# Optimization experiments

Measured on AMD Instinct MI355X. Metric: run time of the kernel, lower is better.

Reference implementation:

```python
import jax, jax.numpy as jnp
import numpy as np
from jax import lax


def _conv(x, w, b):
    # NCHW conv, 3x3, stride 1, SAME padding (matches nn.Conv2d(k=3, padding=1))
    y = lax.conv_general_dilated(x, w, (1, 1), 'SAME',
                                 dimension_numbers=('NCHW', 'OIHW', 'NCHW'))
    return y + b[None, :, None, None]


def _maxpool2(x):
    return lax.reduce_window(x, -jnp.inf, lax.max, (1, 1, 2, 2), (1, 1, 2, 2), 'VALID')


def setup_inputs() -> dict:
    key = jax.random.key(0)
    ks = jax.random.split(key, 8)
    B, C, H, W = 512, 3, 32, 32
    E, NC = 4, 100
    x = jax.random.normal(ks[0], (B, C, H, W), jnp.float32)
    s = lambda k, shape, fan: jax.random.normal(k, shape, jnp.float32) * (1.0 / np.sqrt(fan))
    return {
        'x': x,
        'r_conv_w': s(ks[1], (16, 3, 3, 3), 27),
        'r_conv_b': jnp.zeros((16,), jnp.float32),
        'r_fc_w': s(ks[2], (E, 16), 16),
        'r_fc_b': jnp.zeros((E,), jnp.float32),
        'e_w1': s(ks[3], (E, 32, 3, 3, 3), 27),
        'e_b1': jnp.zeros((E, 32), jnp.float32),
        'e_w2': s(ks[4], (E, 64, 32, 3, 3), 32 * 9),
        'e_b2': jnp.zeros((E, 64), jnp.float32),
        'e_fc_w': s(ks[5], (E, NC, 64 * 8 * 8), 64 * 8 * 8),
        'e_fc_b': jnp.zeros((E, NC), jnp.float32),
        'top_k': 1,
    }


def reference(x, r_conv_w, r_conv_b, r_fc_w, r_fc_b,
              e_w1, e_b1, e_w2, e_b2, e_fc_w, e_fc_b, top_k):
    E = r_fc_w.shape[0]
    # ---- router: conv -> relu -> global avg pool -> linear -> softmax ----
    h = jax.nn.relu(_conv(x, r_conv_w, r_conv_b))
    g = h.mean(axis=(2, 3))                                   # [B, 16]
    router_probs = jax.nn.softmax(g @ r_fc_w.T + r_fc_b, -1)   # [B, E]
    topk_prob, topk_idx = lax.top_k(router_probs, top_k)       # [B, K]

    # ---- experts (dense compute + weighted combine == hard dispatch/combine) ----
    def expert(w1, b1, w2, b2, fw, fb):
        h1 = _maxpool2(jax.nn.relu(_conv(x, w1, b1)))          # [B, 32, 16, 16]
        h2 = _maxpool2(jax.nn.relu(_conv(h1, w2, b2)))         # [B, 64, 8, 8]
        f = h2.reshape(h2.shape[0], -1)                        # [B, 4096]
        return f @ fw.T + fb                                   # [B, NC]

    expert_out = jax.vmap(expert)(e_w1, e_b1, e_w2, e_b2, e_fc_w, e_fc_b)  # [E, B, NC]

    onehot = jax.nn.one_hot(topk_idx, E, dtype=x.dtype)        # [B, K, E]
    comb_w = jnp.einsum('bke,bk->be', onehot, topk_prob)       # [B, E]
    final_output = jnp.einsum('ebc,be->bc', expert_out, comb_w)

    mean_probs = router_probs.mean(axis=0)
    aux_loss = jnp.mean((mean_probs - 1.0 / E) ** 2)
    return final_output, router_probs, aux_loss
```

## Files before the change

kernel.cpp:

```cpp
#include <hip/hip_runtime.h>
#include <hip/hip_bf16.h>
#include <math.h>

#define BATCH 512
#define NC 100

typedef __attribute__((ext_vector_type(8))) short bf16x8;
typedef __attribute__((ext_vector_type(4))) float f32x4;

__device__ inline ushort f2bf(float f) {
    __hip_bfloat16 h = __float2bfloat16(f);
    return *reinterpret_cast<ushort*>(&h);
}

__global__ __launch_bounds__(256) void cvt_all_kernel(const float* __restrict__ fw,
                                                      ushort* __restrict__ fwb,
                                                      const float* __restrict__ w2,
                                                      ushort* __restrict__ w2t,
                                                      const float* __restrict__ w1,
                                                      ushort* __restrict__ w1t)
{
    const int blk = blockIdx.x;
    if (blk < 1600) {
        const int i = (blk * 256 + threadIdx.x) * 4;
        float4 v = *(const float4*)(fw + i);
        ushort o[4];
        o[0] = f2bf(v.x); o[1] = f2bf(v.y); o[2] = f2bf(v.z); o[3] = f2bf(v.w);
        *(uint2*)(fwb + i) = *(uint2*)o;
    } else if (blk < 1888) {
        const int i = (blk - 1600) * 256 + threadIdx.x;
        const int ic = i & 31;
        const int oc = (i >> 5) & 63;
        const int et = i >> 11;
        const int e = et / 9, t = et % 9;
        w2t[i] = f2bf(w2[((e * 64 + oc) * 32 + ic) * 9 + t]);
    } else {
        const int i = (blk - 1888) * 256 + threadIdx.x;
        const int row = i >> 5, k = i & 31;
        w1t[i] = (k < 27) ? f2bf(w1[row * 27 + k]) : (ushort)0;
    }
}

__global__ __launch_bounds__(512) void fused_expert_kernel(
    const float* __restrict__ x,
    const float* __restrict__ rcw,
    const float* __restrict__ rcb,
    const float* __restrict__ rfw,
    const float* __restrict__ rfb,
    const ushort* __restrict__ w1t,
    const float* __restrict__ eb1,
    const ushort* __restrict__ w2t,
    const float* __restrict__ eb2,
    float* __restrict__ probs_out,
    int* __restrict__ sel,
    float* __restrict__ pw,
    uint* __restrict__ h2b)
{
    __shared__ float xs[3 * 34 * 40];
    __shared__ float rcb_s[16];
    __shared__ float rfw_s[68];
    __shared__ float red[8][16];
    __shared__ float g_s[16];
    __shared__ int   sel_s;
    __shared__ float eb1_s[128];
    __shared__ __align__(16) ushort A_s[18 * 18 * 32];

    const int b = blockIdx.x, tid = threadIdx.x;
    const int wvv = tid >> 6, lane = tid & 63;
    const int lr = lane & 15, kb = lane >> 4;

    uint* A32 = (uint*)A_s;
    for (int i = tid; i < 1088; i += 512) {
        int y, xx, w;
        if (i < 576) { y = (i >= 288) ? 17 : 0; int r2 = i % 288; xx = r2 >> 4; w = r2 & 15; }
        else { int j = i - 576; y = 1 + (j >> 5); xx = ((j >> 4) & 1) ? 17 : 0; w = j & 15; }
        A32[(y * 18 + xx) * 16 + w] = 0u;
    }
    for (int i = tid; i < 3 * 34 * 40; i += 512) xs[i] = 0.f;
    if (tid < 128) eb1_s[tid] = eb1[tid];
    if (tid < 68) rfw_s[tid] = (tid < 64) ? rfw[tid] : rfb[tid - 64];
    if (tid >= 128 && tid < 144) rcb_s[tid - 128] = rcb[tid - 128];
    __syncthreads();
    const float* xb = x + b * 3072;
    for (int i = tid; i < 3072; i += 512) {
        int c = i >> 10, r = (i >> 5) & 31, cc = i & 31;
        xs[(c * 34 + r + 1) * 40 + (cc + 1)] = xb[i];
    }
    __syncthreads();

    {
        const int oc = tid & 15, sg = tid >> 4;
        const int pg = sg & 15, half = sg >> 4;
        const int c0 = half * 16;
        float w[27];
#pragma unroll
        for (int j = 0; j < 27; ++j) w[j] = rcw[oc * 27 + j];
        const float bias = rcb_s[oc];
        float a0[16], a1[16];
#pragma unroll
        for (int j = 0; j < 16; ++j) { a0[j] = 0.f; a1[j] = 0.f; }
#pragma unroll
        for (int c = 0; c < 3; ++c) {
#pragma unroll
            for (int ry = 0; ry < 4; ++ry) {
                const float* row = &xs[(c * 34 + 2 * pg + ry) * 40 + c0];
                float rv[18];
                float4 q0 = *(const float4*)(row);
                float4 q1 = *(const float4*)(row + 4);
                float4 q2 = *(const float4*)(row + 8);
                float4 q3 = *(const float4*)(row + 12);
                float2 q4 = *(const float2*)(row + 16);
                rv[0] = q0.x; rv[1] = q0.y; rv[2] = q0.z; rv[3] = q0.w;
                rv[4] = q1.x; rv[5] = q1.y; rv[6] = q1.z; rv[7] = q1.w;
                rv[8] = q2.x; rv[9] = q2.y; rv[10] = q2.z; rv[11] = q2.w;
                rv[12] = q3.x; rv[13] = q3.y; rv[14] = q3.z; rv[15] = q3.w;
                rv[16] = q4.x; rv[17] = q4.y;
                if (ry < 3) {
#pragma unroll
                    for (int kx = 0; kx < 3; ++kx) {
                        const float wv = w[c * 9 + ry * 3 + kx];
#pragma unroll
                        for (int j = 0; j < 16; ++j) a0[j] += wv * rv[j + kx];
                    }
                }
                if (ry > 0) {
#pragma unroll
                    for (int kx = 0; kx < 3; ++kx) {
                        const float wv = w[c * 9 + (ry - 1) * 3 + kx];
#pragma unroll
                        for (int j = 0; j < 16; ++j) a1[j] += wv * rv[j + kx];
                    }
                }
            }
        }
        float accm = 0.f;
#pragma unroll
        for (int j = 0; j < 16; ++j)
            accm += fmaxf(a0[j] + bias, 0.f) + fmaxf(a1[j] + bias, 0.f);
        accm += __shfl_down(accm, 32);
        accm += __shfl_down(accm, 16);
        if (lane < 16) red[wvv][lane] = accm;
    }
    __syncthreads();
    if (tid < 16) {
        float s = 0.f;
#pragma unroll
        for (int w = 0; w < 8; ++w) s += red[w][tid];
        g_s[tid] = s * (1.f / 1024.f);
    }
    __syncthreads();

    if (tid == 0) {
        float logits[4];
#pragma unroll
        for (int e = 0; e < 4; ++e) {
            float s = rfw_s[64 + e];
#pragma unroll
            for (int o = 0; o < 16; ++o) s += g_s[o] * rfw_s[e * 16 + o];
            logits[e] = s;
        }
        float m = fmaxf(fmaxf(logits[0], logits[1]), fmaxf(logits[2], logits[3]));
        float ex[4], ssum = 0.f;
#pragma unroll
        for (int e = 0; e < 4; ++e) { ex[e] = __expf(logits[e] - m); ssum += ex[e]; }
        const float inv = 1.f / ssum;
        float p[4];
#pragma unroll
        for (int e = 0; e < 4; ++e) p[e] = ex[e] * inv;
        int am = 0; float best = p[0];
#pragma unroll
        for (int e = 1; e < 4; ++e) { if (p[e] > best) { best = p[e]; am = e; } }
        *(float4*)(probs_out + b * 4) = make_float4(p[0], p[1], p[2], p[3]);
        sel[b] = am;
        pw[b] = best;
        sel_s = am;
    }
    __syncthreads();
    const int e = sel_s;

    {
        const ushort* bsrc = w1t + (e * 32 + lr) * 32 + kb * 8;
        const bf16x8 b0 = *(const bf16x8*)(bsrc);
        const bf16x8 b1 = *(const bf16x8*)(bsrc + 16 * 32);
        const float bv0 = eb1_s[e * 32 + lr];
        const float bv1 = eb1_s[e * 32 + 16 + lr];

        int offj[8], valj[8];
#pragma unroll
        for (int jj = 0; jj < 8; ++jj) {
            int k = kb * 8 + jj;
            int ic = (k * 57) >> 9; ic = ic > 2 ? 2 : ic;
            int tap = k - ic * 9; tap = tap > 8 ? 8 : tap;
            int ky = (tap * 11) >> 5;
            int kx = tap - ky * 3;
            offj[jj] = (ic * 34 + ky) * 40 + kx;
            valj[jj] = (k < 27);
        }

#pragma unroll 2
        for (int mf = 0; mf < 8; ++mf) {
            const int pA = wvv * 32 + mf * 4 + (lr >> 2);
            const int c2 = lr & 3;
            const int yA = ((pA >> 4) << 1) + (c2 >> 1);
            const int xA = ((pA & 15) << 1) + (c2 & 1);
            const int base = yA * 40 + xA;
            union { uint u[4]; bf16x8 v; } U;
#pragma unroll
            for (int jp = 0; jp < 4; ++jp) {
                float v0 = valj[2 * jp]     ? xs[base + offj[2 * jp]]     : 0.f;
                float v1 = valj[2 * jp + 1] ? xs[base + offj[2 * jp + 1]] : 0.f;
                U.u[jp] = (uint)f2bf(v0) | ((uint)f2bf(v1) << 16);
            }
            const f32x4 z = {0.f, 0.f, 0.f, 0.f};
            f32x4 c0 = __builtin_amdgcn_mfma_f32_16x16x32_bf16(U.v, b0, z, 0, 0, 0);
            f32x4 c1 = __builtin_amdgcn_mfma_f32_16x16x32_bf16(U.v, b1, z, 0, 0, 0);
            const int pp = wvv * 32 + mf * 4 + kb;
            const int py = pp >> 4, px = pp & 15;
            ushort* dst = A_s + ((py + 1) * 18 + (px + 1)) * 32 + lr;
            float m0 = fmaxf(fmaxf(c0[0], c0[1]), fmaxf(c0[2], c0[3]));
            float m1 = fmaxf(fmaxf(c1[0], c1[1]), fmaxf(c1[2], c1[3]));
            dst[0]  = f2bf(fmaxf(m0 + bv0, 0.f));
            dst[16] = f2bf(fmaxf(m1 + bv1, 0.f));
        }
    }
    __syncthreads();

    {
        const int wy = wvv & 3, wn = wvv >> 2;
        const ushort* wgl = w2t + (size_t)e * 18432 + lr * 32 + kb * 8;

        f32x4 acc[4][2];
#pragma unroll
        for (int m = 0; m < 4; ++m)
#pragma unroll
            for (int n = 0; n < 2; ++n)
                acc[m][n] = (f32x4){0.f, 0.f, 0.f, 0.f};

#pragma unroll
        for (int t = 0; t < 9; ++t) {
            const int ky = t / 3, kx = t % 3;
            bf16x8 af[4], bfr[2];
#pragma unroll
            for (int m = 0; m < 4; ++m) {
                const int y = wy * 4 + m;
                af[m] = *(const bf16x8*)(A_s + ((y + ky) * 18 + (lr + kx)) * 32 + kb * 8);
            }
#pragma unroll
            for (int n = 0; n < 2; ++n)
                bfr[n] = *(const bf16x8*)(wgl + (t * 64 + (wn * 2 + n) * 16) * 32);
#pragma unroll
            for (int m = 0; m < 4; ++m)
#pragma unroll
                for (int n = 0; n < 2; ++n)
                    acc[m][n] = __builtin_amdgcn_mfma_f32_16x16x32_bf16(af[m], bfr[n], acc[m][n], 0, 0, 0);
        }

#pragma unroll
        for (int q = 0; q < 2; ++q) {
            const int py = wy * 2 + q;
#pragma unroll
            for (int n = 0; n < 2; ++n) {
                const int oc = (wn * 2 + n) * 16 + lr;
                const float bn = eb2[e * 64 + oc];
                const f32x4 ca = acc[2 * q][n];
                const f32x4 cb = acc[2 * q + 1][n];
                float p0 = fmaxf(fmaxf(ca[0], ca[1]), fmaxf(cb[0], cb[1]));
                float p1 = fmaxf(fmaxf(ca[2], ca[3]), fmaxf(cb[2], cb[3]));
                float r0 = fmaxf(p0 + bn, 0.f);
                float r1 = fmaxf(p1 + bn, 0.f);
                uint pk = (uint)f2bf(r0) | ((uint)f2bf(r1) << 16);
                h2b[(size_t)b * 2048 + oc * 32 + py * 4 + kb] = pk;
            }
        }
    }
}

__global__ __launch_bounds__(512) void scan_aux_kernel(const int* __restrict__ sel,
                                                       const float* __restrict__ probs,
                                                       int* __restrict__ ids,
                                                       int* __restrict__ offs,
                                                       float* __restrict__ aux_out)
{
    __shared__ int wcnt[4][8];
    __shared__ int wbase[4][8];
    __shared__ float wred[8][4];
    const int tid = threadIdx.x;
    const int wv = tid >> 6, lane = tid & 63;
    const int e = sel[tid];
    unsigned long long m[4];
#pragma unroll
    for (int k = 0; k < 4; ++k) m[k] = __ballot(e == k);
    if (lane == 0) {
#pragma unroll
        for (int k = 0; k < 4; ++k) wcnt[k][wv] = __popcll(m[k]);
    }
    float4 p = *(const float4*)(probs + tid * 4);
    float s0 = p.x, s1 = p.y, s2 = p.z, s3 = p.w;
#pragma unroll
    for (int off = 32; off > 0; off >>= 1) {
        s0 += __shfl_down(s0, off);
        s1 += __shfl_down(s1, off);
        s2 += __shfl_down(s2, off);
        s3 += __shfl_down(s3, off);
    }
    if (lane == 0) { wred[wv][0] = s0; wred[wv][1] = s1; wred[wv][2] = s2; wred[wv][3] = s3; }
    __syncthreads();
    if (tid == 0) {
        int o = 0;
        for (int k = 0; k < 4; ++k) {
            offs[k] = o;
            for (int w = 0; w < 8; ++w) { wbase[k][w] = o; o += wcnt[k][w]; }
        }
        offs[4] = o;
        float aux = 0.f;
#pragma unroll
        for (int k = 0; k < 4; ++k) {
            float t = 0.f;
            for (int w = 0; w < 8; ++w) t += wred[w][k];
            float mp = t * (1.f / BATCH) - 0.25f;
            aux += mp * mp;
        }
        aux_out[0] = aux * 0.25f;
    }
    __syncthreads();
    const unsigned long long below = (lane == 0) ? 0ull : (~0ull >> (64 - lane));
    const int rank = __popcll(m[e] & below);
    ids[wbase[e][wv] + rank] = tid;
}

__global__ __launch_bounds__(448) void fc_mfma_kernel(
    const ushort* __restrict__ h2b,
    const ushort* __restrict__ fwb,
    const int* __restrict__ ids,
    const int* __restrict__ offs,
    float* __restrict__ part)
{
    const int mt = blockIdx.x, ks = blockIdx.y, e = blockIdx.z;
    const int off = offs[e], cnt = offs[e + 1] - off;
    if (mt * 16 >= cnt) return;

    const int tid = threadIdx.x;
    const int wv = tid >> 6, lane = tid & 63;
    const int lr = lane & 15, kb = lane >> 4;
    const int cls = wv * 16 + lr;
    const int clsc = cls < NC ? cls : NC - 1;
    const int slot = mt * 16 + lr;
    const int sidx = ids[off + (slot < cnt ? slot : cnt - 1)];

    const ushort* ap = h2b + (size_t)sidx * 4096 + ks * 512 + kb * 8;
    const ushort* bp = fwb + (size_t)(e * NC + clsc) * 4096 + ks * 512 + kb * 8;

    f32x4 acc = {0.f, 0.f, 0.f, 0.f};
#pragma unroll
    for (int k = 0; k < 16; ++k) {
        bf16x8 a = *(const bf16x8*)(ap + k * 32);
        bf16x8 b = *(const bf16x8*)(bp + k * 32);
        acc = __builtin_amdgcn_mfma_f32_16x16x32_bf16(a, b, acc, 0, 0, 0);
    }

    if (cls < NC) {
#pragma unroll
        for (int j = 0; j < 4; ++j) {
            const int m = mt * 16 + kb * 4 + j;
            if (m < cnt) {
                const int sid = ids[off + m];
                part[((size_t)ks * 512 + sid) * NC + cls] = acc[j];
            }
        }
    }
}

__global__ __launch_bounds__(256) void fc_reduce_kernel(
    const float* __restrict__ part,
    const float* __restrict__ fb,
    const int* __restrict__ sel,
    const float* __restrict__ pw,
    float* __restrict__ outp)
{
    const int i = blockIdx.x * 256 + threadIdx.x;
    if (i >= BATCH * NC) return;
    const int s = i / NC, c = i - s * NC;
    float acc = 0.f;
#pragma unroll
    for (int k = 0; k < 8; ++k) acc += part[((size_t)k * 512 + s) * NC + c];
    outp[i] = pw[s] * (acc + fb[sel[s] * NC + c]);
}

extern "C" void kernel_launch(void* const* d_in, const int* in_sizes, int n_in,
                              void* d_out, int out_size, void* d_ws, size_t ws_size,
                              hipStream_t stream) {
    const float* x   = (const float*)d_in[0];
    const float* rcw = (const float*)d_in[1];
    const float* rcb = (const float*)d_in[2];
    const float* rfw = (const float*)d_in[3];
    const float* rfb = (const float*)d_in[4];
    const float* ew1 = (const float*)d_in[5];
    const float* eb1 = (const float*)d_in[6];
    const float* ew2 = (const float*)d_in[7];
    const float* eb2 = (const float*)d_in[8];
    const float* efw = (const float*)d_in[9];
    const float* efb = (const float*)d_in[10];
    (void)in_sizes; (void)n_in; (void)out_size; (void)ws_size;

    float* out       = (float*)d_out;
    float* final_out = out;
    float* probs_out = out + 51200;
    float* aux_out   = out + 53248;

    char* ws = (char*)d_ws;
    int*    sel  = (int*)ws;
    float*  pw   = (float*)(ws + 2048);
    int*    ids  = (int*)(ws + 4096);
    int*    offs = (int*)(ws + 6144);
    uint*   h2b  = (uint*)(ws + 8192);
    ushort* fwb  = (ushort*)(ws + 8192 + 4194304);
    ushort* w2t  = (ushort*)(ws + 8192 + 4194304 + 3276800);
    ushort* w1t  = (ushort*)(ws + 8192 + 4194304 + 3276800 + 147456);
    float*  part = (float*)(ws + 8192 + 4194304 + 3276800 + 147456 + 8192);

    cvt_all_kernel<<<1904, 256, 0, stream>>>(efw, fwb, ew2, w2t, ew1, w1t);
    fused_expert_kernel<<<512, 512, 0, stream>>>(x, rcw, rcb, rfw, rfb, w1t, eb1,
                                                 w2t, eb2, probs_out, sel, pw, h2b);
    scan_aux_kernel<<<1, 512, 0, stream>>>(sel, probs_out, ids, offs, aux_out);
    fc_mfma_kernel<<<dim3(32, 8, 4), 448, 0, stream>>>((const ushort*)h2b, fwb, ids, offs, part);
    fc_reduce_kernel<<<200, 256, 0, stream>>>(part, efb, sel, pw, final_out);
}
```

Before: 42.86 us.

## Compute router conv with split-bf16 MFMA instead of scalar FP32 FMAs

Replaces the scalar FP32 direct convolution in the router with an im2col-style MFMA path. Both weights and input are split into bf16 hi/lo parts, and four bf16 MFMAs emulate near-FP32 accuracy so the top-1 routing decision is preserved. The weight split is precomputed in the conversion kernel with one extra block. The aim is to offload the router's VALU-heavy conv onto matrix cores and reuse the same tap-offset tables as the expert conv, at the cost of extra conversion work per element and slightly different rounding.

```diff
diff --git a/kernel.cpp b/kernel.cpp
--- a/kernel.cpp
+++ b/kernel.cpp
@@ -11,6 +11,10 @@
 __device__ inline ushort f2bf(float f) {
     __hip_bfloat16 h = __float2bfloat16(f);
     return *reinterpret_cast<ushort*>(&h);
+}
+__device__ inline float bf2f(ushort u) {
+    __hip_bfloat16 h = *reinterpret_cast<__hip_bfloat16*>(&u);
+    return __bfloat162float(h);
 }
 
 __global__ __launch_bounds__(256) void cvt_all_kernel(const float* __restrict__ fw,
@@ -18,7 +22,9 @@
                                                       const float* __restrict__ w2,
                                                       ushort* __restrict__ w2t,
                                                       const float* __restrict__ w1,
-                                                      ushort* __restrict__ w1t)
+                                                      ushort* __restrict__ w1t,
+                                                      const float* __restrict__ rcw,
+                                                      ushort* __restrict__ wrt)
 {
     const int blk = blockIdx.x;
     if (blk < 1600) {
@@ -34,16 +40,28 @@
         const int et = i >> 11;
         const int e = et / 9, t = et % 9;
         w2t[i] = f2bf(w2[((e * 64 + oc) * 32 + ic) * 9 + t]);
-    } else {
+    } else if (blk < 1904) {
         const int i = (blk - 1888) * 256 + threadIdx.x;
         const int row = i >> 5, k = i & 31;
         w1t[i] = (k < 27) ? f2bf(w1[row * 27 + k]) : (ushort)0;
+    } else {
+#pragma unroll
+        for (int jj = 0; jj < 4; ++jj) {
+            const int idx = jj * 256 + threadIdx.x;
+            const int part = idx >> 9;
+            const int rem = idx & 511;
+            const int oc = rem >> 5, k = rem & 31;
+            float v = (k < 27) ? rcw[oc * 27 + k] : 0.f;
+            ushort hi = f2bf(v);
+            ushort lo = f2bf(v - bf2f(hi));
+            wrt[idx] = part ? lo : hi;
+        }
     }
 }
 
 __global__ __launch_bounds__(512) void fused_expert_kernel(
     const float* __restrict__ x,
-    const float* __restrict__ rcw,
+    const ushort* __restrict__ wrt,
     const float* __restrict__ rcb,
     const float* __restrict__ rfw,
     const float* __restrict__ rfb,
@@ -88,58 +106,51 @@
     }
     __syncthreads();
 
+    int offj[8], valj[8];
+#pragma unroll
+    for (int jj = 0; jj < 8; ++jj) {
+        int k = kb * 8 + jj;
+        int ic = (k * 57) >> 9; ic = ic > 2 ? 2 : ic;
+        int tap = k - ic * 9; tap = tap > 8 ? 8 : tap;
+        int ky = (tap * 11) >> 5;
+        int kx = tap - ky * 3;
+        offj[jj] = (ic * 34 + ky) * 40 + kx;
+        valj[jj] = (k < 27);
+    }
+
     {
-        const int oc = tid & 15, sg = tid >> 4;
-        const int pg = sg & 15, half = sg >> 4;
-        const int c0 = half * 16;
-        float w[27];
-#pragma unroll
-        for (int j = 0; j < 27; ++j) w[j] = rcw[oc * 27 + j];
-        const float bias = rcb_s[oc];
-        float a0[16], a1[16];
-#pragma unroll
-        for (int j = 0; j < 16; ++j) { a0[j] = 0.f; a1[j] = 0.f; }
-#pragma unroll
-        for (int c = 0; c < 3; ++c) {
-#pragma unroll
-            for (int ry = 0; ry < 4; ++ry) {
-                const float* row = &xs[(c * 34 + 2 * pg + ry) * 40 + c0];
-                float rv[18];
-                float4 q0 = *(const float4*)(row);
-                float4 q1 = *(const float4*)(row + 4);
-                float4 q2 = *(const float4*)(row + 8);
-                float4 q3 = *(const float4*)(row + 12);
-                float2 q4 = *(const float2*)(row + 16);
-                rv[0] = q0.x; rv[1] = q0.y; rv[2] = q0.z; rv[3] = q0.w;
-                rv[4] = q1.x; rv[5] = q1.y; rv[6] = q1.z; rv[7] = q1.w;
-                rv[8] = q2.x; rv[9] = q2.y; rv[10] = q2.z; rv[11] = q2.w;
-                rv[12] = q3.x; rv[13] = q3.y; rv[14] = q3.z; rv[15] = q3.w;
-                rv[16] = q4.x; rv[17] = q4.y;
-                if (ry < 3) {
-#pragma unroll
-                    for (int kx = 0; kx < 3; ++kx) {
-                        const float wv = w[c * 9 + ry * 3 + kx];
-#pragma unroll
-                        for (int j = 0; j < 16; ++j) a0[j] += wv * rv[j + kx];
-                    }
-                }
-                if (ry > 0) {
-#pragma unroll
-                    for (int kx = 0; kx < 3; ++kx) {
-                        const float wv = w[c * 9 + (ry - 1) * 3 + kx];
-#pragma unroll
-                        for (int j = 0; j < 16; ++j) a1[j] += wv * rv[j + kx];
-                    }
-                }
+        const bf16x8 brh = *(const bf16x8*)(wrt + lr * 32 + kb * 8);
+        const bf16x8 brl = *(const bf16x8*)(wrt + 512 + lr * 32 + kb * 8);
+        const float rbias = rcb_s[lr];
+        float racc = 0.f;
+#pragma unroll 2
+        for (int mf = 0; mf < 8; ++mf) {
+            const int pA = wvv * 32 + mf * 4 + (lr >> 2);
+            const int c2 = lr & 3;
+            const int yA = ((pA >> 4) << 1) + (c2 >> 1);
+            const int xA = ((pA & 15) << 1) + (c2 & 1);
+            const int base = yA * 40 + xA;
+            union { uint u[4]; bf16x8 v; } Hi, Lo;
+#pragma unroll
+            for (int jp = 0; jp < 4; ++jp) {
+                float v0 = valj[2 * jp]     ? xs[base + offj[2 * jp]]     : 0.f;
+                float v1 = valj[2 * jp + 1] ? xs[base + offj[2 * jp + 1]] : 0.f;
+                ushort h0 = f2bf(v0), h1 = f2bf(v1);
+                ushort l0 = f2bf(v0 - bf2f(h0)), l1 = f2bf(v1 - bf2f(h1));
+                Hi.u[jp] = (uint)h0 | ((uint)h1 << 16);
+                Lo.u[jp] = (uint)l0 | ((uint)l1 << 16);
             }
-        }
-        float accm = 0.f;
-#pragma unroll
-        for (int j = 0; j < 16; ++j)
-            accm += fmaxf(a0[j] + bias, 0.f) + fmaxf(a1[j] + bias, 0.f);
-        accm += __shfl_down(accm, 32);
-        accm += __shfl_down(accm, 16);
-        if (lane < 16) red[wvv][lane] = accm;
+            f32x4 c = {0.f, 0.f, 0.f, 0.f};
+            c = __builtin_amdgcn_mfma_f32_16x16x32_bf16(Lo.v, brl, c, 0, 0, 0);
+            c = __builtin_amdgcn_mfma_f32_16x16x32_bf16(Lo.v, brh, c, 0, 0, 0);
+            c = __builtin_amdgcn_mfma_f32_16x16x32_bf16(Hi.v, brl, c, 0, 0, 0);
+            c = __builtin_amdgcn_mfma_f32_16x16x32_bf16(Hi.v, brh, c, 0, 0, 0);
+#pragma unroll
+            for (int j = 0; j < 4; ++j) racc += fmaxf(c[j] + rbias, 0.f);
+        }
+        racc += __shfl_down(racc, 32);
+        racc += __shfl_down(racc, 16);
+        if (lane < 16) red[wvv][lane] = racc;
     }
     __syncthreads();
     if (tid < 16) {
@@ -184,18 +195,6 @@
         const bf16x8 b1 = *(const bf16x8*)(bsrc + 16 * 32);
         const float bv0 = eb1_s[e * 32 + lr];
         const float bv1 = eb1_s[e * 32 + 16 + lr];
-
-        int offj[8], valj[8];
-#pragma unroll
-        for (int jj = 0; jj < 8; ++jj) {
-            int k = kb * 8 + jj;
-            int ic = (k * 57) >> 9; ic = ic > 2 ? 2 : ic;
-            int tap = k - ic * 9; tap = tap > 8 ? 8 : tap;
-            int ky = (tap * 11) >> 5;
-            int kx = tap - ky * 3;
-            offj[jj] = (ic * 34 + ky) * 40 + kx;
-            valj[jj] = (k < 27);
-        }
 
 #pragma unroll 2
         for (int mf = 0; mf < 8; ++mf) {
@@ -416,10 +415,11 @@
     ushort* fwb  = (ushort*)(ws + 8192 + 4194304);
     ushort* w2t  = (ushort*)(ws + 8192 + 4194304 + 3276800);
     ushort* w1t  = (ushort*)(ws + 8192 + 4194304 + 3276800 + 147456);
-    float*  part = (float*)(ws + 8192 + 4194304 + 3276800 + 147456 + 8192);
-
-    cvt_all_kernel<<<1904, 256, 0, stream>>>(efw, fwb, ew2, w2t, ew1, w1t);
-    fused_expert_kernel<<<512, 512, 0, stream>>>(x, rcw, rcb, rfw, rfb, w1t, eb1,
+    ushort* wrt  = (ushort*)(ws + 8192 + 4194304 + 3276800 + 147456 + 8192);
+    float*  part = (float*)(ws + 8192 + 4194304 + 3276800 + 147456 + 8192 + 2048);
+
+    cvt_all_kernel<<<1905, 256, 0, stream>>>(efw, fwb, ew2, w2t, ew1, w1t, rcw, wrt);
+    fused_expert_kernel<<<512, 512, 0, stream>>>(x, wrt, rcb, rfw, rfb, w1t, eb1,
                                                  w2t, eb2, probs_out, sel, pw, h2b);
     scan_aux_kernel<<<1, 512, 0, stream>>>(sel, probs_out, ids, offs, aux_out);
     fc_mfma_kernel<<<dim3(32, 8, 4), 448, 0, stream>>>((const ushort*)h2b, fwb, ids, offs, part);
```

Result: no change. 43.05 us (+0.5%).
